# Optimization experiments

Hardware: AMD Instinct MI355X
Metric: run time of the kernel (lower is better)

Reference implementation:

```python
import jax, jax.numpy as jnp
import numpy as np
import math

R, C, B, E, H, F = 64, 256, 1, 768, 12, 3072
D = E // H  # head dim = 64
EPS = 1e-6  # flax LayerNorm default


def _ln(x, s, b):
    mu = jnp.mean(x, axis=-1, keepdims=True)
    var = jnp.mean((x - mu) ** 2, axis=-1, keepdims=True)
    return (x - mu) * jax.lax.rsqrt(var + EPS) * s + b


def setup_inputs() -> dict:
    key = jax.random.key(0)
    ks = jax.random.split(key, 16)
    w = lambda k, sh: jax.random.normal(k, sh, jnp.float32) * 0.02
    z = lambda sh: jnp.zeros(sh, jnp.float32)
    return {
        "x": jax.random.normal(ks[0], (R, C, B, E), jnp.float32),
        "ln1_s": jnp.ones((E,), jnp.float32), "ln1_b": z((E,)),
        "r_wq": w(ks[1], (E, E)), "r_bq": z((E,)),
        "r_wk": w(ks[2], (E, E)), "r_bk": z((E,)),
        "r_wv": w(ks[3], (E, E)), "r_bv": z((E,)),
        "r_wo": w(ks[4], (E, E)), "r_bo": z((E,)),
        "ln2_s": jnp.ones((E,), jnp.float32), "ln2_b": z((E,)),
        "c_wq": w(ks[5], (E, E)), "c_bq": z((E,)),
        "c_wk": w(ks[6], (E, E)), "c_bk": z((E,)),
        "c_wv": w(ks[7], (E, E)), "c_bv": z((E,)),
        "c_wo": w(ks[8], (E, E)), "c_bo": z((E,)),
        "ln3_s": jnp.ones((E,), jnp.float32), "ln3_b": z((E,)),
        "f_w1": w(ks[9], (E, F)), "f_b1": z((F,)),
        "f_w2": w(ks[10], (F, E)), "f_b2": z((E,)),
    }


def reference(x, ln1_s, ln1_b, r_wq, r_bq, r_wk, r_bk, r_wv, r_bv, r_wo, r_bo,
              ln2_s, ln2_b, c_wq, c_bq, c_wk, c_bk, c_wv, c_bv, c_wo, c_bo,
              ln3_s, ln3_b, f_w1, f_b1, f_w2, f_b2):
    qkv = (R, C, B, H, D)
    # --- tied row self-attention (NOTE: original code has no residual adds) ---
    h = _ln(x, ln1_s, ln1_b)
    q = (h @ r_wq + r_bq).reshape(qkv) * (D ** -0.5 / math.sqrt(R))  # tied-row scaling
    k = (h @ r_wk + r_bk).reshape(qkv)
    v = (h @ r_wv + r_bv).reshape(qkv)
    aw = jnp.einsum('rinhd,rjnhd->hnij', q, k)  # single softmax tied across rows
    ap = jax.nn.softmax(aw, axis=-1)
    ctx = jnp.einsum('hnij,rjnhd->rinhd', ap, v).reshape(R, C, B, E)
    x = ctx @ r_wo + r_bo
    # --- column self-attention (per-column attention over rows) ---
    h = _ln(x, ln2_s, ln2_b)
    q = (h @ c_wq + c_bq).reshape(qkv) * (D ** -0.5)
    k = (h @ c_wk + c_bk).reshape(qkv)
    v = (h @ c_wv + c_bv).reshape(qkv)
    aw = jnp.einsum('icnhd,jcnhd->hcnij', q, k)
    ap = jax.nn.softmax(aw, axis=-1)
    ctx = jnp.einsum('hcnij,jcnhd->icnhd', ap, v).reshape(R, C, B, E)
    x = ctx @ c_wo + c_bo
    # --- FFN (gelu approximate=True matches flax default) ---
    h = _ln(x, ln3_s, ln3_b)
    return jax.nn.gelu(h @ f_w1 + f_b1) @ f_w2 + f_b2
```

## Files before the change

kernel.cpp:

```cpp
#include <hip/hip_runtime.h>
#include <hip/hip_bf16.h>
#include <stdint.h>
#include <stddef.h>

#define R_ 64
#define C_ 256
#define E_ 768
#define H_ 12
#define F_ 3072
#define D_ 64
#define NT_ (R_*C_)
#define HCRD_ ((size_t)H_*C_*R_*D_)

typedef float f32x4 __attribute__((ext_vector_type(4)));
typedef __bf16 bf16x8 __attribute__((ext_vector_type(8)));
typedef unsigned short us4 __attribute__((ext_vector_type(4)));
typedef unsigned short us8 __attribute__((ext_vector_type(8)));

typedef __attribute__((address_space(3))) uint32_t lds_u32;
typedef __attribute__((address_space(1))) uint32_t glb_u32;

__device__ __forceinline__ void gld16(const uint16_t* g, uint16_t* l) {
  __builtin_amdgcn_global_load_lds((const glb_u32*)g, (lds_u32*)l, 16, 0, 0);
}

__device__ __forceinline__ uint16_t f2b(float f) {
  __bf16 h = (__bf16)f;
  return *(uint16_t*)&h;
}

enum { EP_F32B = 0, EP_GELU = 1, EP_AW = 2, EP_CTX = 3, EP_QKVROW = 4, EP_QKVCOL = 5 };

template<int EP, bool SWZ, bool PERM>
__global__ __launch_bounds__(256)
void gemm_bt(const uint16_t* __restrict__ A, const uint16_t* __restrict__ B,
             const float* __restrict__ bias, const float* __restrict__ biasK,
             const float* __restrict__ biasV, void* __restrict__ out,
             int M, int N, int K, int lda, int ldb, long sAz, long sBz, float scale)
{
  __shared__ uint16_t As[2][128 * 32];
  __shared__ uint16_t Bs[2][128 * 32];
  const int tid  = threadIdx.x;
  const int wave = tid >> 6, lane = tid & 63;
  const int z = blockIdx.z;

  int bx = blockIdx.x, by = blockIdx.y;
  if constexpr (SWZ) {
    int lin = blockIdx.x + gridDim.x * blockIdx.y;
    const int q = (gridDim.x * gridDim.y) >> 3;
    const int wid = (lin & 7) * q + (lin >> 3);
    bx = wid % gridDim.x; by = wid / gridDim.x;
  }

  const long bm = (long)by * 128;
  int kc = 0; long bnb = bx;
  if constexpr (EP == EP_AW) { kc = bx & 3; bnb = bx >> 2; }
  const long bn = bnb * 128;
  const uint16_t* Bb = B + (long)z * sBz + bn * (long)ldb + (long)kc * 1024;
  const int wr = (wave >> 1) * 64;
  const int wc = (wave & 1) * 64;
  const int lr = lane & 15;
  const int lq = lane >> 4;

  const int t0 = tid, t1 = tid + 256;
  const int ar0 = t0 >> 2, ac0 = (t0 & 3) * 8;
  const int ar1 = t1 >> 2, ac1 = (t1 & 3) * 8;

  long am0 = bm + ar0, am1 = bm + ar1;
  if constexpr (PERM) {
    am0 = ((am0 & 63) << 8) | (am0 >> 6);
    am1 = ((am1 & 63) << 8) | (am1 >> 6);
  }
  const uint16_t* a0p = A + (long)z * sAz + am0 * (long)lda + (long)kc * 1024;
  const uint16_t* a1p = A + (long)z * sAz + am1 * (long)lda + (long)kc * 1024;
  const uint16_t* b0p = Bb + (long)ar0 * ldb;
  const uint16_t* b1p = Bb + (long)ar1 * ldb;

  auto STAGE = [&](int bi, int kt) {
    gld16(a0p + kt + ac0, &As[bi][t0 * 8]);
    gld16(a1p + kt + ac1, &As[bi][t1 * 8]);
    gld16(b0p + kt + ac0, &Bs[bi][t0 * 8]);
    gld16(b1p + kt + ac1, &Bs[bi][t1 * 8]);
  };

  f32x4 acc[4][4];
#pragma unroll
  for (int i = 0; i < 4; ++i)
#pragma unroll
    for (int j = 0; j < 4; ++j) acc[i][j] = (f32x4){0.f, 0.f, 0.f, 0.f};

  const int nt = K >> 5;
  STAGE(0, 0);
  __syncthreads();
  int cur = 0;
  for (int t = 0; t < nt; ++t) {
    if (t + 1 < nt) STAGE(cur ^ 1, (t + 1) << 5);

    bf16x8 af[4], bfm[4];
#pragma unroll
    for (int i = 0; i < 4; ++i) {
      af[i]  = *(const bf16x8*)&As[cur][(wr + i * 16 + lr) * 32 + lq * 8];
      bfm[i] = *(const bf16x8*)&Bs[cur][(wc + i * 16 + lr) * 32 + lq * 8];
    }
#pragma unroll
    for (int mi = 0; mi < 4; ++mi)
#pragma unroll
      for (int ni = 0; ni < 4; ++ni)
        acc[mi][ni] = __builtin_amdgcn_mfma_f32_16x16x32_bf16(af[mi], bfm[ni], acc[mi][ni], 0, 0, 0);

    __syncthreads();
    cur ^= 1;
  }

  if constexpr (EP == EP_F32B) {
#pragma unroll
    for (int mi = 0; mi < 4; ++mi)
#pragma unroll
      for (int ni = 0; ni < 4; ++ni)
#pragma unroll
        for (int r = 0; r < 4; ++r) {
          const long row = bm + wr + mi * 16 + lq * 4 + r;
          const long col = bn + wc + ni * 16 + lr;
          ((float*)out)[row * N + col] = acc[mi][ni][r] + bias[col];
        }
  } else if constexpr (EP == EP_AW) {
#pragma unroll
    for (int mi = 0; mi < 4; ++mi)
#pragma unroll
      for (int ni = 0; ni < 4; ++ni)
#pragma unroll
        for (int r = 0; r < 4; ++r) {
          const long row = bm + wr + mi * 16 + lq * 4 + r;
          const long col = bn + wc + ni * 16 + lr;
          ((float*)out)[((long)(z * 4 + kc) * M + row) * N + col] = acc[mi][ni][r];
        }
  } else if constexpr (EP == EP_CTX) {
#pragma unroll
    for (int mi = 0; mi < 4; ++mi)
#pragma unroll
      for (int ni = 0; ni < 4; ++ni)
#pragma unroll
        for (int r = 0; r < 4; ++r) {
          const long row = bm + wr + mi * 16 + lq * 4 + r;
          const long col = bn + wc + ni * 16 + lr;
          ((uint16_t*)out)[((col >> 6) * C_ + row) * E_ + (long)z * 64 + (col & 63)] =
              f2b(acc[mi][ni][r]);
        }
  } else {
    uint16_t* slab = (wave < 2) ? &As[wave][0] : &Bs[wave - 2][0];
    const long colb = bn + wc;
    int grp = 0; long cc0 = colb;
    const float* bb = bias;
    if constexpr (EP != EP_GELU) {
      grp = colb >= 1536 ? 2 : (colb >= 768 ? 1 : 0);
      cc0 = colb - (long)grp * 768;
      bb = grp == 0 ? bias : (grp == 1 ? biasK : biasV);
    }
    const bool tr = (EP != EP_GELU) && (grp == 2);

#pragma unroll
    for (int mi = 0; mi < 4; ++mi)
#pragma unroll
      for (int ni = 0; ni < 4; ++ni)
#pragma unroll
        for (int r = 0; r < 4; ++r) {
          const int lrow = mi * 16 + lq * 4 + r;
          const int lcol = ni * 16 + lr;
          float val;
          if constexpr (EP == EP_GELU) {
            const float t = acc[mi][ni][r] + bias[colb + lcol];
            const float u = 0.7978845608028654f * (t + 0.044715f * t * t * t);
            const float e = __expf(2.f * u);
            val = 0.5f * t * (2.f - 2.f / (e + 1.f));
          } else {
            val = acc[mi][ni][r] + bb[cc0 + lcol];
            if (grp == 0) val *= scale;
          }
          const int sr = tr ? lcol : lrow;
          const int sc = tr ? lrow : lcol;
          const int psc = (sc & 7) | ((((sc >> 3) ^ (sr & 7))) << 3);
          slab[sr * 64 + psc] = f2b(val);
        }

    uint16_t* o16 = (uint16_t*)out;
    long obase, rstride;
    if constexpr (EP == EP_GELU) {
      obase = (bm + wr) * (long)N + colb; rstride = N;
    } else {
      const long h = cc0 >> 6;
      const long m0 = bm + wr;
      if constexpr (EP == EP_QKVROW) {
        const long rr = m0 >> 8, c0 = m0 & 255;
        if (grp < 2) { obase = (size_t)grp * HCRD_ + ((h * C_ + c0) * R_ + rr) * D_; rstride = R_ * D_; }
        else         { obase = 2 * HCRD_ + ((h * R_ + rr) * D_) * C_ + c0;           rstride = C_; }
      } else {
        const long cq = m0 >> 6;
        if (grp < 2) { obase = (size_t)grp * HCRD_ + ((h * C_ + cq) * R_) * D_; rstride = D_; }
        else         { obase = 2 * HCRD_ + ((h * C_ + cq) * D_) * R_;           rstride = R_; }
      }
    }

    const int rl = lane >> 3, chn = lane & 7;
#pragma unroll
    for (int pp = 0; pp < 8; ++pp) {
      const int srow = pp * 8 + rl;
      const int pch = chn ^ (srow & 7);
      us8 wv = *(const us8*)&slab[srow * 64 + pch * 8];
      *(us8*)(o16 + obase + (long)srow * rstride + chn * 8) = wv;
    }
  }
}

__global__ __launch_bounds__(256)
void ln_k(const float* __restrict__ x, const float* __restrict__ s, const float* __restrict__ b,
          uint16_t* __restrict__ out)
{
  const int wave = threadIdx.x >> 6, lane = threadIdx.x & 63;
  const long row = (long)blockIdx.x * 4 + wave;
  const float* xr = x + row * E_;
  f32x4 v[3];
  float sum = 0.f, sq = 0.f;
#pragma unroll
  for (int i = 0; i < 3; ++i) {
    v[i] = *(const f32x4*)(xr + (i * 64 + lane) * 4);
#pragma unroll
    for (int j = 0; j < 4; ++j) { sum += v[i][j]; sq += v[i][j] * v[i][j]; }
  }
#pragma unroll
  for (int m = 1; m < 64; m <<= 1) { sum += __shfl_xor(sum, m); sq += __shfl_xor(sq, m); }
  const float mu = sum * (1.f / E_);
  const float var = sq * (1.f / E_) - mu * mu;
  const float rs = rsqrtf(var + 1e-6f);
  uint16_t* orow = out + row * E_;
#pragma unroll
  for (int i = 0; i < 3; ++i) {
    const int e0 = (i * 64 + lane) * 4;
    us4 o;
#pragma unroll
    for (int j = 0; j < 4; ++j) o[j] = f2b((v[i][j] - mu) * rs * s[e0 + j] + b[e0 + j]);
    *(us4*)(orow + e0) = o;
  }
}

__global__ __launch_bounds__(256)
void softmax_k4(const float* __restrict__ aw4, uint16_t* __restrict__ ap)
{
  const int wave = threadIdx.x >> 6, lane = threadIdx.x & 63;
  const long row = (long)blockIdx.x * 4 + wave;
  const long h = row >> 8, i = row & 255;
  f32x4 v = (f32x4){0.f, 0.f, 0.f, 0.f};
#pragma unroll
  for (int kc = 0; kc < 4; ++kc) {
    f32x4 t = *(const f32x4*)(aw4 + (((h * 4 + kc) * C_ + i) * C_) + lane * 4);
#pragma unroll
    for (int j = 0; j < 4; ++j) v[j] += t[j];
  }
  float m = fmaxf(fmaxf(v[0], v[1]), fmaxf(v[2], v[3]));
#pragma unroll
  for (int k = 1; k < 64; k <<= 1) m = fmaxf(m, __shfl_xor(m, k));
  f32x4 e; float s = 0.f;
#pragma unroll
  for (int j = 0; j < 4; ++j) { e[j] = __expf(v[j] - m); s += e[j]; }
#pragma unroll
  for (int k = 1; k < 64; k <<= 1) s += __shfl_xor(s, k);
  const float inv = 1.f / s;
  us4 o;
#pragma unroll
  for (int j = 0; j < 4; ++j) o[j] = f2b(e[j] * inv);
  *(us4*)(ap + row * C_ + lane * 4) = o;
}

__global__ __launch_bounds__(256)
void tcvt(const float* __restrict__ in, uint16_t* __restrict__ out, int K, int N)
{
  __shared__ float t[32][33];
  const int tx = threadIdx.x, ty = threadIdx.y;
  const long k0 = (long)blockIdx.y * 32, n0 = (long)blockIdx.x * 32;
  for (int i = ty; i < 32; i += 8) t[i][tx] = in[(k0 + i) * N + n0 + tx];
  __syncthreads();
  for (int i = ty; i < 32; i += 8) out[(n0 + i) * K + k0 + tx] = f2b(t[tx][i]);
}

__global__ __launch_bounds__(64)
void colattn(const uint16_t* __restrict__ q, const uint16_t* __restrict__ k,
             const uint16_t* __restrict__ v, uint16_t* __restrict__ ctx)
{
  __shared__ uint16_t Qs[64 * 64];
  __shared__ uint16_t Ks[64 * 64];
  __shared__ uint16_t Vs[64 * 64];
  const int hc = blockIdx.x;
  const int h = hc >> 8, c = hc & 255;
  const int lane = threadIdx.x;
  const uint16_t* qb = q + (long)hc * (R_ * D_);
  const uint16_t* kb = k + (long)hc * (R_ * D_);
  const uint16_t* vb = v + (long)hc * (D_ * R_);
#pragma unroll
  for (int it = 0; it < 8; ++it) {
    const int o = (it * 64 + lane) * 8;
    gld16(qb + o, &Qs[o]);
    gld16(kb + o, &Ks[o]);
    gld16(vb + o, &Vs[o]);
  }
  asm volatile("s_waitcnt vmcnt(0)" ::: "memory");
  __builtin_amdgcn_sched_barrier(0);

  const int lr = lane & 15, lq = lane >> 4;
  f32x4 acc[4][4];
#pragma unroll
  for (int i = 0; i < 4; ++i)
#pragma unroll
    for (int j = 0; j < 4; ++j) acc[i][j] = (f32x4){0.f, 0.f, 0.f, 0.f};

#pragma unroll
  for (int kt = 0; kt < 2; ++kt) {
    bf16x8 af[4], bfm[4];
#pragma unroll
    for (int i = 0; i < 4; ++i) {
      af[i]  = *(const bf16x8*)&Qs[(i * 16 + lr) * 64 + kt * 32 + lq * 8];
      bfm[i] = *(const bf16x8*)&Ks[(i * 16 + lr) * 64 + kt * 32 + lq * 8];
    }
#pragma unroll
    for (int mi = 0; mi < 4; ++mi)
#pragma unroll
      for (int ni = 0; ni < 4; ++ni)
        acc[mi][ni] = __builtin_amdgcn_mfma_f32_16x16x32_bf16(af[mi], bfm[ni], acc[mi][ni], 0, 0, 0);
  }

#pragma unroll
  for (int mi = 0; mi < 4; ++mi) {
#pragma unroll
    for (int r = 0; r < 4; ++r) {
      float mx = fmaxf(fmaxf(acc[mi][0][r], acc[mi][1][r]), fmaxf(acc[mi][2][r], acc[mi][3][r]));
#pragma unroll
      for (int s = 1; s < 16; s <<= 1) mx = fmaxf(mx, __shfl_xor(mx, s));
      float e0 = __expf(acc[mi][0][r] - mx), e1 = __expf(acc[mi][1][r] - mx);
      float e2 = __expf(acc[mi][2][r] - mx), e3 = __expf(acc[mi][3][r] - mx);
      float sum = e0 + e1 + e2 + e3;
#pragma unroll
      for (int s = 1; s < 16; s <<= 1) sum += __shfl_xor(sum, s);
      const float inv = 1.f / sum;
      const int i = mi * 16 + lq * 4 + r;
      Qs[i * 64 +  0 + lr] = f2b(e0 * inv);
      Qs[i * 64 + 16 + lr] = f2b(e1 * inv);
      Qs[i * 64 + 32 + lr] = f2b(e2 * inv);
      Qs[i * 64 + 48 + lr] = f2b(e3 * inv);
    }
  }
  __syncthreads();

  f32x4 o_[4][4];
#pragma unroll
  for (int i = 0; i < 4; ++i)
#pragma unroll
    for (int j = 0; j < 4; ++j) o_[i][j] = (f32x4){0.f, 0.f, 0.f, 0.f};

#pragma unroll
  for (int kt = 0; kt < 2; ++kt) {
    bf16x8 pa[4], vv[4];
#pragma unroll
    for (int i = 0; i < 4; ++i) {
      pa[i] = *(const bf16x8*)&Qs[(i * 16 + lr) * 64 + kt * 32 + lq * 8];
      vv[i] = *(const bf16x8*)&Vs[(i * 16 + lr) * 64 + kt * 32 + lq * 8];
    }
#pragma unroll
    for (int mi = 0; mi < 4; ++mi)
#pragma unroll
      for (int ni = 0; ni < 4; ++ni)
        o_[mi][ni] = __builtin_amdgcn_mfma_f32_16x16x32_bf16(pa[mi], vv[ni], o_[mi][ni], 0, 0, 0);
  }

#pragma unroll
  for (int mi = 0; mi < 4; ++mi)
#pragma unroll
    for (int ni = 0; ni < 4; ++ni)
#pragma unroll
      for (int r = 0; r < 4; ++r) {
        const int i = mi * 16 + lq * 4 + r;
        const int d = ni * 16 + lr;
        ctx[((long)i * C_ + c) * E_ + h * 64 + d] = f2b(o_[mi][ni][r]);
      }
}

extern "C" void kernel_launch(void* const* d_in, const int* in_sizes, int n_in,
                              void* d_out, int out_size, void* d_ws, size_t ws_size,
                              hipStream_t stream)
{
  (void)in_sizes; (void)n_in; (void)out_size; (void)ws_size;
  const float* x     = (const float*)d_in[0];
  const float* ln1_s = (const float*)d_in[1];
  const float* ln1_b = (const float*)d_in[2];
  const float* r_wq  = (const float*)d_in[3];
  const float* r_bq  = (const float*)d_in[4];
  const float* r_wk  = (const float*)d_in[5];
  const float* r_bk  = (const float*)d_in[6];
  const float* r_wv  = (const float*)d_in[7];
  const float* r_bv  = (const float*)d_in[8];
  const float* r_wo  = (const float*)d_in[9];
  const float* r_bo  = (const float*)d_in[10];
  const float* ln2_s = (const float*)d_in[11];
  const float* ln2_b = (const float*)d_in[12];
  const float* c_wq  = (const float*)d_in[13];
  const float* c_bq  = (const float*)d_in[14];
  const float* c_wk  = (const float*)d_in[15];
  const float* c_bk  = (const float*)d_in[16];
  const float* c_wv  = (const float*)d_in[17];
  const float* c_bv  = (const float*)d_in[18];
  const float* c_wo  = (const float*)d_in[19];
  const float* c_bo  = (const float*)d_in[20];
  const float* ln3_s = (const float*)d_in[21];
  const float* ln3_b = (const float*)d_in[22];
  const float* f_w1  = (const float*)d_in[23];
  const float* f_b1  = (const float*)d_in[24];
  const float* f_w2  = (const float*)d_in[25];
  const float* f_b2  = (const float*)d_in[26];

  uint8_t* p = (uint8_t*)d_ws;
  auto take = [&p](size_t n) { uint8_t* r = p; p += (n + 255) & ~(size_t)255; return r; };

  uint16_t* wqkv1 = (uint16_t*)take((size_t)3 * E_ * E_ * 2);
  uint16_t* wqkv2 = (uint16_t*)take((size_t)3 * E_ * E_ * 2);
  uint16_t* rwoT  = (uint16_t*)take((size_t)E_ * E_ * 2);
  uint16_t* cwoT  = (uint16_t*)take((size_t)E_ * E_ * 2);
  uint16_t* w1T   = (uint16_t*)take((size_t)E_ * F_ * 2);
  uint16_t* w2T   = (uint16_t*)take((size_t)F_ * E_ * 2);
  uint16_t* hb    = (uint16_t*)take((size_t)NT_ * E_ * 2);
  uint16_t* qkvT  = (uint16_t*)take(3 * HCRD_ * 2);
  uint16_t* qT = qkvT, *kT = qkvT + HCRD_, *vT = qkvT + 2 * HCRD_;
  uint16_t* ctxb  = (uint16_t*)take((size_t)NT_ * E_ * 2);
  uint16_t* apb   = (uint16_t*)take((size_t)H_ * C_ * C_ * 2);
  uint16_t* g     = qkvT;
  float*    awb4  = (float*)ctxb;
  float*    x1    = (float*)d_out;

  const dim3 tb32(32, 8);
  const dim3 gEE(E_ / 32, E_ / 32);
  tcvt<<<gEE, tb32, 0, stream>>>(r_wq, wqkv1 + 0 * E_ * E_, E_, E_);
  tcvt<<<gEE, tb32, 0, stream>>>(r_wk, wqkv1 + 1 * E_ * E_, E_, E_);
  tcvt<<<gEE, tb32, 0, stream>>>(r_wv, wqkv1 + 2 * E_ * E_, E_, E_);
  tcvt<<<gEE, tb32, 0, stream>>>(c_wq, wqkv2 + 0 * E_ * E_, E_, E_);
  tcvt<<<gEE, tb32, 0, stream>>>(c_wk, wqkv2 + 1 * E_ * E_, E_, E_);
  tcvt<<<gEE, tb32, 0, stream>>>(c_wv, wqkv2 + 2 * E_ * E_, E_, E_);
  tcvt<<<gEE, tb32, 0, stream>>>(r_wo, rwoT, E_, E_);
  tcvt<<<gEE, tb32, 0, stream>>>(c_wo, cwoT, E_, E_);
  tcvt<<<dim3(F_ / 32, E_ / 32), tb32, 0, stream>>>(f_w1, w1T, E_, F_);
  tcvt<<<dim3(E_ / 32, F_ / 32), tb32, 0, stream>>>(f_w2, w2T, F_, E_);

  const dim3 gProj(E_ / 128, NT_ / 128, 1);
  const dim3 gQKV((3 * E_) / 128, NT_ / 128, 1);

  ln_k<<<NT_ / 4, 256, 0, stream>>>(x, ln1_s, ln1_b, hb);
  gemm_bt<EP_QKVROW, true, false><<<gQKV, 256, 0, stream>>>(hb, wqkv1, r_bq, r_bk, r_bv, qkvT,
      NT_, 3 * E_, E_, E_, E_, 0, 0, 0.015625f);
  gemm_bt<EP_AW, false, false><<<dim3(8, C_ / 128, H_), 256, 0, stream>>>(
      qT, kT, nullptr, nullptr, nullptr, awb4,
      C_, C_, 1024, R_ * D_, R_ * D_, (long)C_ * R_ * D_, (long)C_ * R_ * D_, 1.f);
  softmax_k4<<<(H_ * C_) / 4, 256, 0, stream>>>(awb4, apb);
  gemm_bt<EP_CTX, false, false><<<dim3((R_ * D_) / 128, C_ / 128, H_), 256, 0, stream>>>(
      apb, vT, nullptr, nullptr, nullptr,
      ctxb, C_, R_ * D_, C_, C_, C_, (long)C_ * C_, (long)R_ * D_ * C_, 1.f);
  gemm_bt<EP_F32B, true, false><<<gProj, 256, 0, stream>>>(ctxb, rwoT, r_bo, nullptr, nullptr, x1,
      NT_, E_, E_, E_, E_, 0, 0, 1.f);

  ln_k<<<NT_ / 4, 256, 0, stream>>>(x1, ln2_s, ln2_b, hb);
  gemm_bt<EP_QKVCOL, true, true><<<gQKV, 256, 0, stream>>>(hb, wqkv2, c_bq, c_bk, c_bv, qkvT,
      NT_, 3 * E_, E_, E_, E_, 0, 0, 0.125f);
  colattn<<<H_ * C_, 64, 0, stream>>>(qT, kT, vT, ctxb);
  gemm_bt<EP_F32B, true, false><<<gProj, 256, 0, stream>>>(ctxb, cwoT, c_bo, nullptr, nullptr, x1,
      NT_, E_, E_, E_, E_, 0, 0, 1.f);

  ln_k<<<NT_ / 4, 256, 0, stream>>>(x1, ln3_s, ln3_b, hb);
  gemm_bt<EP_GELU, true, false><<<dim3(F_ / 128, NT_ / 128, 1), 256, 0, stream>>>(
      hb, w1T, f_b1, nullptr, nullptr, g,
      NT_, F_, E_, E_, E_, 0, 0, 1.f);
  gemm_bt<EP_F32B, true, false><<<gProj, 256, 0, stream>>>(g, w2T, f_b2, nullptr, nullptr, d_out,
      NT_, E_, F_, F_, F_, 0, 0, 1.f);
}
```

Measured before the change: 598.4 us.

## Triple-buffer GEMM LDS staging with XOR swizzle and vmcnt-based waits

The generic bf16 GEMM moves from a double-buffered LDS pipeline to a triple-buffered one that prefetches two k-tiles ahead. It replaces __syncthreads with explicit vmcnt waits plus raw barriers, so loads for the next-next tile can stay in flight during compute. It also XOR-swizzles the 16-byte column chunks in LDS to cut bank conflicts on fragment reads, and raises wave priority around the MFMA block. The cost is 50% more LDS per block, which may reduce occupancy, and the hand-placed waits must stay correct against the async global_load_lds traffic.

After: 596.6 us. No clear change (-0.3%).

```diff
diff --git a/kernel.cpp b/kernel.cpp
--- a/kernel.cpp
+++ b/kernel.cpp
@@ -29,6 +29,10 @@
   return *(uint16_t*)&h;
 }
 
+#define VM_WAIT4 { asm volatile("s_waitcnt vmcnt(4)" ::: "memory"); __builtin_amdgcn_sched_barrier(0); }
+#define VM_WAIT0 { asm volatile("s_waitcnt vmcnt(0)" ::: "memory"); __builtin_amdgcn_sched_barrier(0); }
+#define BARRIER  { __builtin_amdgcn_s_barrier(); __builtin_amdgcn_sched_barrier(0); }
+
 enum { EP_F32B = 0, EP_GELU = 1, EP_AW = 2, EP_CTX = 3, EP_QKVROW = 4, EP_QKVCOL = 5 };
 
 template<int EP, bool SWZ, bool PERM>
@@ -38,8 +42,8 @@
              const float* __restrict__ biasV, void* __restrict__ out,
              int M, int N, int K, int lda, int ldb, long sAz, long sBz, float scale)
 {
-  __shared__ uint16_t As[2][128 * 32];
-  __shared__ uint16_t Bs[2][128 * 32];
+  __shared__ uint16_t As[3][4096];
+  __shared__ uint16_t Bs[3][4096];
   const int tid  = threadIdx.x;
   const int wave = tid >> 6, lane = tid & 63;
   const int z = blockIdx.z;
@@ -63,8 +67,9 @@
   const int lq = lane >> 4;
 
   const int t0 = tid, t1 = tid + 256;
-  const int ar0 = t0 >> 2, ac0 = (t0 & 3) * 8;
-  const int ar1 = t1 >> 2, ac1 = (t1 & 3) * 8;
+  const int ar0 = t0 >> 2, ar1 = t1 >> 2;
+  const int ac0 = (((t0 & 3) ^ ((ar0 >> 1) & 3)) * 8);
+  const int ac1 = (((t1 & 3) ^ ((ar1 >> 1) & 3)) * 8);
 
   long am0 = bm + ar0, am1 = bm + ar1;
   if constexpr (PERM) {
@@ -83,6 +88,15 @@
     gld16(b1p + kt + ac1, &Bs[bi][t1 * 8]);
   };
 
+  int apos[4], bpos[4];
+#pragma unroll
+  for (int i = 0; i < 4; ++i) {
+    const int ra = wr + i * 16 + lr;
+    const int rb = wc + i * 16 + lr;
+    apos[i] = ra * 32 + (lq ^ ((ra >> 1) & 3)) * 8;
+    bpos[i] = rb * 32 + (lq ^ ((rb >> 1) & 3)) * 8;
+  }
+
   f32x4 acc[4][4];
 #pragma unroll
   for (int i = 0; i < 4; ++i)
@@ -91,26 +105,35 @@
 
   const int nt = K >> 5;
   STAGE(0, 0);
-  __syncthreads();
+  if (nt > 1) { STAGE(1, 32); VM_WAIT4; } else { VM_WAIT0; }
+  BARRIER;
+
   int cur = 0;
   for (int t = 0; t < nt; ++t) {
-    if (t + 1 < nt) STAGE(cur ^ 1, (t + 1) << 5);
+    if (t + 2 < nt) {
+      int sl = cur + 2; if (sl >= 3) sl -= 3;
+      STAGE(sl, (t + 2) << 5);
+    }
 
     bf16x8 af[4], bfm[4];
 #pragma unroll
     for (int i = 0; i < 4; ++i) {
-      af[i]  = *(const bf16x8*)&As[cur][(wr + i * 16 + lr) * 32 + lq * 8];
-      bfm[i] = *(const bf16x8*)&Bs[cur][(wc + i * 16 + lr) * 32 + lq * 8];
-    }
+      af[i]  = *(const bf16x8*)&As[cur][apos[i]];
+      bfm[i] = *(const bf16x8*)&Bs[cur][bpos[i]];
+    }
+    __builtin_amdgcn_s_setprio(1);
 #pragma unroll
     for (int mi = 0; mi < 4; ++mi)
 #pragma unroll
       for (int ni = 0; ni < 4; ++ni)
         acc[mi][ni] = __builtin_amdgcn_mfma_f32_16x16x32_bf16(af[mi], bfm[ni], acc[mi][ni], 0, 0, 0);
-
-    __syncthreads();
-    cur ^= 1;
-  }
+    __builtin_amdgcn_s_setprio(0);
+
+    if (t + 2 < nt)      { VM_WAIT4; BARRIER; }
+    else if (t + 1 < nt) { VM_WAIT0; BARRIER; }
+    cur = (cur == 2) ? 0 : cur + 1;
+  }
+  __syncthreads();
 
   if constexpr (EP == EP_F32B) {
 #pragma unroll
@@ -147,7 +170,7 @@
               f2b(acc[mi][ni][r]);
         }
   } else {
-    uint16_t* slab = (wave < 2) ? &As[wave][0] : &Bs[wave - 2][0];
+    uint16_t* slab = (wave < 3) ? &As[wave][0] : &Bs[0][0];
     const long colb = bn + wc;
     int grp = 0; long cc0 = colb;
     const float* bb = bias;
```
